# Optimization experiments

Measured on AMD Instinct MI355X. Metric: run time of the kernel, lower is better.

The kernel has to match this reference:

```python
import jax, jax.numpy as jnp
import numpy as np

D_MODEL, N_HEADS, D_FF = 768, 12, 3072
B, S = 2, 2048
EPS = 1e-6

def _ln(x, alpha, bias):
    # Matches torch: std with Bessel correction (unbiased), scalar alpha/bias
    mean = x.mean(axis=-1, keepdims=True)
    std = jnp.std(x, axis=-1, keepdims=True, ddof=1)
    return alpha * (x - mean) / (std + EPS) + bias

def setup_inputs() -> dict:
    key = jax.random.key(0)
    ks = jax.random.split(key, 12)
    def w(k, shp):
        return jax.random.normal(k, shp, dtype=jnp.float32) * 0.02
    inp = {
        "x": jax.random.normal(ks[0], (B, S, D_MODEL), dtype=jnp.float32),
        "mask": jnp.ones((B, 1, 1, S), dtype=jnp.int32),
        "wq": w(ks[1], (D_MODEL, D_MODEL)), "bq": jnp.zeros((D_MODEL,), jnp.float32),
        "wk": w(ks[2], (D_MODEL, D_MODEL)), "bk": jnp.zeros((D_MODEL,), jnp.float32),
        "wv": w(ks[3], (D_MODEL, D_MODEL)), "bv": jnp.zeros((D_MODEL,), jnp.float32),
        "wo": w(ks[4], (D_MODEL, D_MODEL)), "bo": jnp.zeros((D_MODEL,), jnp.float32),
        "w1": w(ks[5], (D_MODEL, D_FF)), "b1": jnp.zeros((D_FF,), jnp.float32),
        "w2": w(ks[6], (D_FF, D_MODEL)), "b2": jnp.zeros((D_MODEL,), jnp.float32),
        "ln1_a": jnp.ones((1,), jnp.float32), "ln1_b": jnp.zeros((1,), jnp.float32),
        "ln2_a": jnp.ones((1,), jnp.float32), "ln2_b": jnp.zeros((1,), jnp.float32),
    }
    return inp

def reference(x, mask, wq, bq, wk, bk, wv, bv, wo, bo, w1, b1, w2, b2,
              ln1_a, ln1_b, ln2_a, ln2_b):
    d_k = D_MODEL // N_HEADS
    # --- residual 1: pre-LN self-attention ---
    h = _ln(x, ln1_a, ln1_b)
    q = (h @ wq + bq).reshape(B, S, N_HEADS, d_k).transpose(0, 2, 1, 3)
    k = (h @ wk + bk).reshape(B, S, N_HEADS, d_k).transpose(0, 2, 1, 3)
    v = (h @ wv + bv).reshape(B, S, N_HEADS, d_k).transpose(0, 2, 1, 3)
    scores = jnp.einsum('bhqd,bhkd->bhqk', q, k) / jnp.sqrt(jnp.float32(d_k))
    scores = jnp.where(mask == 0, jnp.float32(-1e9), scores)
    attn = jax.nn.softmax(scores, axis=-1)            # [B,H,S,S] materialized, as in source
    ctx = jnp.einsum('bhqk,bhkd->bhqd', attn, v)
    ctx = ctx.transpose(0, 2, 1, 3).reshape(B, S, D_MODEL)
    x = x + (ctx @ wo + bo)
    # --- residual 2: pre-LN FFN ---
    h = _ln(x, ln2_a, ln2_b)
    ffn = jax.nn.relu(h @ w1 + b1) @ w2 + b2
    return x + ffn
```

## Files before the change

kernel.cpp:

```cpp
#include <hip/hip_runtime.h>
#include <math.h>

#define DM    768
#define NH    12
#define DKH   64
#define DFF   3072
#define BATCH 2
#define SLEN  2048
#define MTOT  4096
#define LNEPS 1e-6f
#define QSCALE 0.18033688011112042f

typedef unsigned short u16;
typedef __attribute__((ext_vector_type(8))) short bf16x8;
typedef __attribute__((ext_vector_type(4))) float f32x4;
typedef __attribute__((ext_vector_type(4))) unsigned short us4;

__device__ __forceinline__ u16 f2bf(float f) {
    union { float f; unsigned int u; } v; v.f = f;
    unsigned int r = v.u + 0x7FFFu + ((v.u >> 16) & 1u);
    return (u16)(r >> 16);
}

__device__ __forceinline__ unsigned pk2bf_t(float lo, float hi) {
    union { float f; unsigned u; } a, b;
    a.f = lo; b.f = hi;
    return __builtin_amdgcn_perm(b.u, a.u, 0x07060302u);
}

__device__ __forceinline__ void gld16(const void* g, void* lds) {
    __builtin_amdgcn_global_load_lds(
        (const __attribute__((address_space(1))) unsigned int*)(unsigned long long)g,
        (__attribute__((address_space(3))) unsigned int*)(unsigned int)(unsigned long long)lds,
        16, 0, 0);
}

__global__ __launch_bounds__(256) void ln_kernel(const float* __restrict__ x,
                                                 u16* __restrict__ out,
                                                 const float* __restrict__ alpha_p,
                                                 const float* __restrict__ beta_p,
                                                 const float* __restrict__ b2,
                                                 float* __restrict__ out2) {
    int row = blockIdx.x;
    const float* xr = x + (size_t)row * DM;
    int t = threadIdx.x;
    float v0 = xr[t], v1 = xr[t + 256], v2 = xr[t + 512];
    float s = v0 + v1 + v2;
    #pragma unroll
    for (int off = 32; off > 0; off >>= 1) s += __shfl_down(s, off);
    __shared__ float red[4], red2[4];
    int wv = t >> 6, ln = t & 63;
    if (ln == 0) red[wv] = s;
    __syncthreads();
    float mean = (red[0] + red[1] + red[2] + red[3]) * (1.0f / 768.0f);
    float d0 = v0 - mean, d1 = v1 - mean, d2 = v2 - mean;
    float sq = d0 * d0 + d1 * d1 + d2 * d2;
    #pragma unroll
    for (int off = 32; off > 0; off >>= 1) sq += __shfl_down(sq, off);
    if (ln == 0) red2[wv] = sq;
    __syncthreads();
    float var = (red2[0] + red2[1] + red2[2] + red2[3]) * (1.0f / 767.0f);
    float scale = alpha_p[0] / (sqrtf(var) + LNEPS);
    float bias = beta_p[0];
    u16* orow = out + (size_t)row * DM;
    orow[t]       = f2bf(d0 * scale + bias);
    orow[t + 256] = f2bf(d1 * scale + bias);
    orow[t + 512] = f2bf(d2 * scale + bias);
    if (out2) {
        float* o2 = out2 + (size_t)row * DM;
        o2[t]       = v0 + b2[t];
        o2[t + 256] = v1 + b2[t + 256];
        o2[t + 512] = v2 + b2[t + 512];
    }
}

__global__ __launch_bounds__(256) void wcast_all(
        const float* __restrict__ wq, const float* __restrict__ wk,
        const float* __restrict__ wv, const float* __restrict__ wo,
        const float* __restrict__ w1, const float* __restrict__ w2,
        u16* __restrict__ wqT, u16* __restrict__ wkT, u16* __restrict__ wvT,
        u16* __restrict__ woT, u16* __restrict__ w1T, u16* __restrict__ w2T) {
    __shared__ float tile[32][33];
    int bid = blockIdx.x;
    const float* src; u16* dst; int R, C, bx, by;
    if (bid < 2304) {
        int j = bid / 576, tix = bid % 576;
        R = 768; C = 768; bx = tix % 24; by = tix / 24;
        src = (j == 0) ? wq : (j == 1) ? wk : (j == 2) ? wv : wo;
        dst = (j == 0) ? wqT : (j == 1) ? wkT : (j == 2) ? wvT : woT;
    } else if (bid < 4608) {
        int tix = bid - 2304;
        R = 768; C = 3072; bx = tix % 96; by = tix / 96;
        src = w1; dst = w1T;
    } else {
        int tix = bid - 4608;
        R = 3072; C = 768; bx = tix % 24; by = tix / 24;
        src = w2; dst = w2T;
    }
    int t = threadIdx.x, tx = t & 31, ty = t >> 5;
    int r0 = by * 32, c0 = bx * 32;
    #pragma unroll
    for (int p = 0; p < 4; p++)
        tile[ty + p * 8][tx] = src[(size_t)(r0 + ty + p * 8) * C + c0 + tx];
    __syncthreads();
    #pragma unroll
    for (int p = 0; p < 4; p++)
        dst[(size_t)(c0 + ty + p * 8) * R + r0 + tx] = f2bf(tile[tx][ty + p * 8]);
}

template<int EPI>
__device__ __forceinline__ void gemm128_core(const u16* __restrict__ A,
                                             const u16* __restrict__ Wt,
                                             const float* __restrict__ bias,
                                             const float* __restrict__ resid,
                                             void* __restrict__ Cout,
                                             int M, int N, int Kstride, int Kloop,
                                             float scale, int bm, int bn) {
    __shared__ __align__(16) u16 As[2][128 * 32];
    __shared__ __align__(16) u16 Bs[2][128 * 32];
    int t = threadIdx.x;
    int ln = t & 63, w = t >> 6;
    int wm = w >> 1, wn = w & 1;
    int quad = ln >> 4, col = ln & 15;
    int m0 = bm * 128, n0 = bn * 128;

    f32x4 acc[4][4];
    const f32x4 zero = {0.f, 0.f, 0.f, 0.f};
    #pragma unroll
    for (int i = 0; i < 4; i++)
        #pragma unroll
        for (int j = 0; j < 4; j++) acc[i][j] = zero;

    int st_ch = (((ln & 3) ^ ((ln >> 3) & 3))) * 8;
    const u16* Ag = A  + (size_t)(m0 + 32 * w + (ln >> 2)) * Kstride + st_ch;
    const u16* Bg = Wt + (size_t)(n0 + 32 * w + (ln >> 2)) * Kstride + st_ch;

    gld16(Ag,                As[0] + w * 1024);
    gld16(Ag + 16 * Kstride, As[0] + w * 1024 + 512);
    gld16(Bg,                Bs[0] + w * 1024);
    gld16(Bg + 16 * Kstride, Bs[0] + w * 1024 + 512);
    __syncthreads();

    int rch = (quad ^ ((col >> 1) & 3)) * 8;

    for (int k0 = 0; k0 < Kloop; k0 += 32) {
        int cur = (k0 >> 5) & 1, nxt = cur ^ 1;
        if (k0 + 32 < Kloop) {
            gld16(Ag + k0 + 32,                As[nxt] + w * 1024);
            gld16(Ag + k0 + 32 + 16 * Kstride, As[nxt] + w * 1024 + 512);
            gld16(Bg + k0 + 32,                Bs[nxt] + w * 1024);
            gld16(Bg + k0 + 32 + 16 * Kstride, Bs[nxt] + w * 1024 + 512);
        }
        bf16x8 af[4], bfr[4];
        #pragma unroll
        for (int i = 0; i < 4; i++)
            af[i] = *(const bf16x8*)&As[cur][(wm * 64 + i * 16 + col) * 32 + rch];
        #pragma unroll
        for (int j = 0; j < 4; j++)
            bfr[j] = *(const bf16x8*)&Bs[cur][(wn * 64 + j * 16 + col) * 32 + rch];
        #pragma unroll
        for (int i = 0; i < 4; i++)
            #pragma unroll
            for (int j = 0; j < 4; j++)
                acc[i][j] = __builtin_amdgcn_mfma_f32_16x16x32_bf16(af[i], bfr[j], acc[i][j], 0, 0, 0);
        __syncthreads();
    }

    #pragma unroll
    for (int i = 0; i < 4; i++) {
        int mb = m0 + wm * 64 + i * 16 + quad * 4;
        #pragma unroll
        for (int j = 0; j < 4; j++) {
            int n = n0 + wn * 64 + j * 16 + col;
            if (EPI == 0 || EPI == 1) {
                float bs = bias[n];
                u16* Cb = (u16*)Cout;
                #pragma unroll
                for (int r = 0; r < 4; r++) {
                    float f = (acc[i][j][r] + bs) * ((EPI == 0) ? scale : 1.0f);
                    if (EPI == 1) f = fmaxf(f, 0.f);
                    Cb[(size_t)(mb + r) * N + n] = f2bf(f);
                }
            } else if (EPI == 2) {
                float bs = bias[n];
                float* Cf = (float*)Cout;
                #pragma unroll
                for (int r = 0; r < 4; r++)
                    Cf[(size_t)(mb + r) * N + n] =
                        acc[i][j][r] + bs + resid[(size_t)(mb + r) * N + n];
            } else if (EPI == 3) {
                float bs = bias[n];
                u16* Cb = (u16*)Cout;
                us4 pk;
                #pragma unroll
                for (int r = 0; r < 4; r++) pk[r] = f2bf(acc[i][j][r] + bs);
                *(us4*)&Cb[(size_t)n * M + mb] = pk;
            } else {
                float* Cf = (float*)Cout;
                #pragma unroll
                for (int r = 0; r < 4; r++)
                    atomicAdd(&Cf[(size_t)(mb + r) * N + n], acc[i][j][r]);
            }
        }
    }
}

template<int EPI>
__global__ __launch_bounds__(256) void gemm_kernel(const u16* __restrict__ A,
                                                   const u16* __restrict__ Wt,
                                                   const float* __restrict__ bias,
                                                   const float* __restrict__ resid,
                                                   void* __restrict__ C,
                                                   int M, int N, int Kstride, int Kloop,
                                                   float scale) {
    const u16* Az = A  + (size_t)blockIdx.z * Kloop;
    const u16* Wz = Wt + (size_t)blockIdx.z * Kloop;
    gemm128_core<EPI>(Az, Wz, bias, resid, C, M, N, Kstride, Kloop, scale,
                      blockIdx.y, blockIdx.x);
}

__global__ __launch_bounds__(256) void qkv_kernel(const u16* __restrict__ h,
        const u16* __restrict__ wqT, const u16* __restrict__ wkT, const u16* __restrict__ wvT,
        const float* __restrict__ bq, const float* __restrict__ bk, const float* __restrict__ bv,
        u16* __restrict__ q, u16* __restrict__ k, u16* __restrict__ vT) {
    int z = blockIdx.z;
    if (z == 0)      gemm128_core<0>(h, wqT, bq, nullptr, q,  MTOT, DM, DM, DM, QSCALE, blockIdx.y, blockIdx.x);
    else if (z == 1) gemm128_core<0>(h, wkT, bk, nullptr, k,  MTOT, DM, DM, DM, 1.0f,   blockIdx.y, blockIdx.x);
    else             gemm128_core<3>(h, wvT, bv, nullptr, vT, MTOT, DM, DM, DM, 1.0f,   blockIdx.y, blockIdx.x);
}

template<int EPI>
__global__ __launch_bounds__(256) void gemm64_kernel(const u16* __restrict__ A,
                                                     const u16* __restrict__ Wt,
                                                     const float* __restrict__ bias,
                                                     const float* __restrict__ resid,
                                                     void* __restrict__ Cout,
                                                     int M, int N, int Kstride, int Kloop) {
    __shared__ __align__(16) u16 As[2][64 * 32];
    __shared__ __align__(16) u16 Bs[2][64 * 32];
    int t = threadIdx.x, ln = t & 63, w = t >> 6;
    int wm = w >> 1, wn = w & 1;
    int quad = ln >> 4, col = ln & 15;
    int m0 = blockIdx.y * 64, n0 = blockIdx.x * 64;

    f32x4 acc[2][2];
    const f32x4 zero = {0.f, 0.f, 0.f, 0.f};
    #pragma unroll
    for (int i = 0; i < 2; i++)
        #pragma unroll
        for (int j = 0; j < 2; j++) acc[i][j] = zero;

    int st_ch = (((ln & 3) ^ ((ln >> 3) & 3))) * 8;
    const u16* Ag = A  + (size_t)(m0 + 16 * w + (ln >> 2)) * Kstride + st_ch;
    const u16* Bg = Wt + (size_t)(n0 + 16 * w + (ln >> 2)) * Kstride + st_ch;
    gld16(Ag, As[0] + w * 512);
    gld16(Bg, Bs[0] + w * 512);
    __syncthreads();

    int rch = (quad ^ ((col >> 1) & 3)) * 8;

    for (int k0 = 0; k0 < Kloop; k0 += 32) {
        int cur = (k0 >> 5) & 1, nxt = cur ^ 1;
        if (k0 + 32 < Kloop) {
            gld16(Ag + k0 + 32, As[nxt] + w * 512);
            gld16(Bg + k0 + 32, Bs[nxt] + w * 512);
        }
        bf16x8 af[2], bfr[2];
        #pragma unroll
        for (int i = 0; i < 2; i++)
            af[i] = *(const bf16x8*)&As[cur][(wm * 32 + i * 16 + col) * 32 + rch];
        #pragma unroll
        for (int j = 0; j < 2; j++)
            bfr[j] = *(const bf16x8*)&Bs[cur][(wn * 32 + j * 16 + col) * 32 + rch];
        #pragma unroll
        for (int i = 0; i < 2; i++)
            #pragma unroll
            for (int j = 0; j < 2; j++)
                acc[i][j] = __builtin_amdgcn_mfma_f32_16x16x32_bf16(af[i], bfr[j], acc[i][j], 0, 0, 0);
        __syncthreads();
    }

    #pragma unroll
    for (int i = 0; i < 2; i++) {
        int mb = m0 + wm * 32 + i * 16 + quad * 4;
        #pragma unroll
        for (int j = 0; j < 2; j++) {
            int n = n0 + wn * 32 + j * 16 + col;
            float bs = bias[n];
            float* Cf = (float*)Cout;
            #pragma unroll
            for (int r = 0; r < 4; r++)
                Cf[(size_t)(mb + r) * N + n] =
                    acc[i][j][r] + bs + resid[(size_t)(mb + r) * N + n];
        }
    }
}

__global__ __launch_bounds__(256) void attn_kernel(const u16* __restrict__ qg,
                                                   const u16* __restrict__ kg,
                                                   const u16* __restrict__ vTg,
                                                   const int* __restrict__ mask,
                                                   u16* __restrict__ ctx) {
    __shared__ __align__(16) u16 Qs[64 * 64];
    __shared__ __align__(16) u16 KV[4][64 * 64];
    __shared__ __align__(16) u16 Ps[4][32 * 40];
    __shared__ __align__(16) float Msf[2][64];
    __shared__ float Lp[64][2];
    int t = threadIdx.x, ln = t & 63, w = t >> 6;
    int quad = ln >> 4, col = ln & 15;
    int qh = w >> 1, kh = w & 1;
    int bh = blockIdx.x, qb = blockIdx.y;
    int b = bh / NH, h = bh - b * NH;
    int q0 = qb * 64;
    size_t qkbase = ((size_t)b * SLEN) * DM + h * DKH;
    size_t vbase  = ((size_t)h * DKH) * MTOT + (size_t)b * SLEN;

    int sw_st = (((ln & 7) ^ (ln >> 3)) * 8);

    {
        const u16* g0 = qg + qkbase + (size_t)(q0 + 16 * w + (ln >> 3)) * DM + sw_st;
        gld16(g0,          Qs + w * 1024);
        gld16(g0 + 8 * DM, Qs + w * 1024 + 512);
        const u16* kg0 = kg + qkbase + (size_t)(16 * w + (ln >> 3)) * DM + sw_st;
        gld16(kg0,          KV[0] + w * 1024);
        gld16(kg0 + 8 * DM, KV[0] + w * 1024 + 512);
        const u16* vg0 = vTg + vbase + (size_t)(16 * w + (ln >> 3)) * MTOT + sw_st;
        gld16(vg0,            KV[2] + w * 1024);
        gld16(vg0 + 8 * MTOT, KV[2] + w * 1024 + 512);
        if (t < 64) Msf[0][t] = mask[b * SLEN + t] ? 0.f : -1e9f;
    }
    __syncthreads();

    bf16x8 bqf[2][2];
    #pragma unroll
    for (int qgi = 0; qgi < 2; qgi++) {
        int rq = qh * 32 + qgi * 16 + col;
        int cq = ((quad ^ (rq & 7)) * 8);
        bqf[qgi][0] = *(const bf16x8*)&Qs[rq * 64 + cq];
        bqf[qgi][1] = *(const bf16x8*)&Qs[rq * 64 + (cq ^ 32)];
    }

    const u16* kpn = kg + qkbase + (size_t)(64 + 16 * w + (ln >> 3)) * DM + sw_st;
    const u16* vpn = vTg + vbase + (size_t)(16 * w + (ln >> 3)) * MTOT + 64 + sw_st;
    const int* mpn = mask + b * SLEN + 64 + t;

    float lacc[2] = {0.f, 0.f};
    f32x4 Ov[2][4];
    const f32x4 zero = {0.f, 0.f, 0.f, 0.f};
    #pragma unroll
    for (int qgi = 0; qgi < 2; qgi++)
        #pragma unroll
        for (int dg = 0; dg < 4; dg++) Ov[qgi][dg] = zero;
    u16* Psw = &Ps[w][0];

    for (int j0 = 0; j0 < SLEN; j0 += 64) {
        int cur = (j0 >> 6) & 1, nxt = cur ^ 1;
        if (j0 + 64 < SLEN) {
            gld16(kpn,            KV[nxt] + w * 1024);
            gld16(kpn + 8 * DM,   KV[nxt] + w * 1024 + 512);
            gld16(vpn,            KV[2 + nxt] + w * 1024);
            gld16(vpn + 8 * MTOT, KV[2 + nxt] + w * 1024 + 512);
            if (t < 64) Msf[nxt][t] = *mpn ? 0.f : -1e9f;
            kpn += 64 * DM; vpn += 64; mpn += 64;
        }

        bf16x8 ak[2][2];
        #pragma unroll
        for (int kgi = 0; kgi < 2; kgi++) {
            int rk = kh * 32 + kgi * 16 + col;
            int ck = ((quad ^ (rk & 7)) * 8);
            ak[kgi][0] = *(const bf16x8*)&KV[cur][rk * 64 + ck];
            ak[kgi][1] = *(const bf16x8*)&KV[cur][rk * 64 + (ck ^ 32)];
        }
        #pragma unroll
        for (int kgi = 0; kgi < 2; kgi++) {
            f32x4 bias4 = *(const f32x4*)&Msf[cur][kh * 32 + kgi * 16 + quad * 4];
            #pragma unroll
            for (int qgi = 0; qgi < 2; qgi++) {
                f32x4 S = __builtin_amdgcn_mfma_f32_16x16x32_bf16(ak[kgi][0], bqf[qgi][0], bias4, 0, 0, 0);
                S       = __builtin_amdgcn_mfma_f32_16x16x32_bf16(ak[kgi][1], bqf[qgi][1], S,     0, 0, 0);
                float p0 = exp2f(S[0]), p1 = exp2f(S[1]);
                float p2 = exp2f(S[2]), p3 = exp2f(S[3]);
                lacc[qgi] += (p0 + p1) + (p2 + p3);
                uint2 pk;
                pk.x = pk2bf_t(p0, p1);
                pk.y = pk2bf_t(p2, p3);
                *(uint2*)&Psw[(qgi * 16 + col) * 40 + kgi * 16 + quad * 4] = pk;
            }
        }
        bf16x8 ap[2];
        #pragma unroll
        for (int qgi = 0; qgi < 2; qgi++)
            ap[qgi] = *(const bf16x8*)&Psw[(qgi * 16 + col) * 40 + quad * 8];
        #pragma unroll
        for (int dg = 0; dg < 4; dg++) {
            int rv = dg * 16 + col;
            int cv = (((kh * 4 + quad) ^ (rv & 7)) * 8);
            bf16x8 bv = *(const bf16x8*)&KV[2 + cur][rv * 64 + cv];
            Ov[0][dg] = __builtin_amdgcn_mfma_f32_16x16x32_bf16(ap[0], bv, Ov[0][dg], 0, 0, 0);
            Ov[1][dg] = __builtin_amdgcn_mfma_f32_16x16x32_bf16(ap[1], bv, Ov[1][dg], 0, 0, 0);
        }
        __syncthreads();
    }

    #pragma unroll
    for (int qgi = 0; qgi < 2; qgi++) {
        lacc[qgi] += __shfl_xor(lacc[qgi], 16);
        lacc[qgi] += __shfl_xor(lacc[qgi], 32);
        if (quad == 0) Lp[qh * 32 + qgi * 16 + col][kh] = lacc[qgi];
    }
    float* Osh = (float*)&KV[0][0];
    if (kh == 1) {
        #pragma unroll
        for (int qgi = 0; qgi < 2; qgi++)
            #pragma unroll
            for (int dg = 0; dg < 4; dg++)
                *(f32x4*)&Osh[(qh * 64 + dg * 16 + col) * 36 + qgi * 16 + quad * 4] = Ov[qgi][dg];
    }
    __syncthreads();
    if (kh == 0) {
        #pragma unroll
        for (int qgi = 0; qgi < 2; qgi++) {
            float linv[4];
            #pragma unroll
            for (int r = 0; r < 4; r++) {
                int ql = qh * 32 + qgi * 16 + quad * 4 + r;
                linv[r] = 1.0f / (Lp[ql][0] + Lp[ql][1]);
            }
            #pragma unroll
            for (int dg = 0; dg < 4; dg++) {
                f32x4 oo = *(const f32x4*)&Osh[(qh * 64 + dg * 16 + col) * 36 + qgi * 16 + quad * 4];
                #pragma unroll
                for (int r = 0; r < 4; r++) {
                    int qrow = q0 + qh * 32 + qgi * 16 + quad * 4 + r;
                    ctx[qkbase + (size_t)qrow * DM + dg * 16 + col] =
                        f2bf((Ov[qgi][dg][r] + oo[r]) * linv[r]);
                }
            }
        }
    }
}

extern "C" void kernel_launch(void* const* d_in, const int* in_sizes, int n_in,
                              void* d_out, int out_size, void* d_ws, size_t ws_size,
                              hipStream_t stream) {
    const float* x    = (const float*)d_in[0];
    const int*   mask = (const int*)d_in[1];
    const float* wq   = (const float*)d_in[2];
    const float* bq   = (const float*)d_in[3];
    const float* wk   = (const float*)d_in[4];
    const float* bk   = (const float*)d_in[5];
    const float* wv   = (const float*)d_in[6];
    const float* bv   = (const float*)d_in[7];
    const float* wo   = (const float*)d_in[8];
    const float* bo   = (const float*)d_in[9];
    const float* w1   = (const float*)d_in[10];
    const float* b1   = (const float*)d_in[11];
    const float* w2   = (const float*)d_in[12];
    const float* b2   = (const float*)d_in[13];
    const float* ln1a = (const float*)d_in[14];
    const float* ln1b = (const float*)d_in[15];
    const float* ln2a = (const float*)d_in[16];
    const float* ln2b = (const float*)d_in[17];
    float* out = (float*)d_out;

    char* w8 = (char*)d_ws;
    u16*   ffn = (u16*)(w8 + 0);
    u16*   q   = (u16*)(w8 + 0);
    u16*   kb  = (u16*)(w8 + 6291456);
    u16*   vT  = (u16*)(w8 + 12582912);
    u16*   ctx = (u16*)(w8 + 18874368);
    u16*   h   = (u16*)(w8 + 25165824);
    float* x1  = (float*)(w8 + 31457280);
    u16*   wqT = (u16*)(w8 + 44040192);
    u16*   wkT = (u16*)(w8 + 45219840);
    u16*   wvT = (u16*)(w8 + 46399488);
    u16*   woT = (u16*)(w8 + 47579136);
    u16*   w1T = (u16*)(w8 + 48758784);
    u16*   w2T = (u16*)(w8 + 53477376);

    wcast_all<<<6912, 256, 0, stream>>>(wq, wk, wv, wo, w1, w2,
                                        wqT, wkT, wvT, woT, w1T, w2T);
    ln_kernel<<<MTOT, 256, 0, stream>>>(x, h, ln1a, ln1b, nullptr, nullptr);
    qkv_kernel<<<dim3(6, 32, 3), 256, 0, stream>>>(h, wqT, wkT, wvT, bq, bk, bv, q, kb, vT);
    attn_kernel<<<dim3(BATCH * NH, SLEN / 64), 256, 0, stream>>>(q, kb, vT, mask, ctx);
    gemm64_kernel<2><<<dim3(12, 64), 256, 0, stream>>>(ctx, woT, bo, x, (void*)x1,
                                                       MTOT, DM, DM, DM);
    ln_kernel<<<MTOT, 256, 0, stream>>>(x1, h, ln2a, ln2b, b2, out);
    gemm_kernel<1><<<dim3(24, 32), 256, 0, stream>>>(h, w1T, b1, nullptr, (void*)ffn,
                                                     MTOT, DFF, DM, DM, 1.0f);
    gemm_kernel<5><<<dim3(6, 32, 2), 256, 0, stream>>>(ffn, w2T, nullptr, nullptr, (void*)out,
                                                       MTOT, DM, DFF, DFF / 2, 1.0f);
}
```

Measured before the change: 294.6 us.

## Shrink all GEMM tiles to 64x64, fuse LN1 into weight prep, MFMA row sums

Replaces the 128x128 GEMM core with a 64x64 core for the QKV, FFN1 and FFN2 GEMMs, quadrupling block counts to raise occupancy and CU coverage at the cost of lower per-block data reuse. Merges the first LayerNorm launch into the weight-cast kernel to save a launch. In attention, the softmax denominator is accumulated with an MFMA against a ones vector instead of scalar adds and shuffles, offloading VALU work onto the matrix unit.

```diff
diff --git a/kernel.cpp b/kernel.cpp
--- a/kernel.cpp
+++ b/kernel.cpp
@@ -35,13 +35,12 @@
         16, 0, 0);
 }
 
-__global__ __launch_bounds__(256) void ln_kernel(const float* __restrict__ x,
-                                                 u16* __restrict__ out,
-                                                 const float* __restrict__ alpha_p,
-                                                 const float* __restrict__ beta_p,
-                                                 const float* __restrict__ b2,
-                                                 float* __restrict__ out2) {
-    int row = blockIdx.x;
+__device__ __forceinline__ void ln_body(const float* __restrict__ x,
+                                        u16* __restrict__ out,
+                                        const float* __restrict__ alpha_p,
+                                        const float* __restrict__ beta_p,
+                                        const float* __restrict__ b2,
+                                        float* __restrict__ out2, int row) {
     const float* xr = x + (size_t)row * DM;
     int t = threadIdx.x;
     float v0 = xr[t], v1 = xr[t + 256], v2 = xr[t + 512];
@@ -74,14 +73,44 @@
     }
 }
 
-__global__ __launch_bounds__(256) void wcast_all(
+__global__ __launch_bounds__(256) void ln_kernel(const float* __restrict__ x,
+                                                 u16* __restrict__ out,
+                                                 const float* __restrict__ alpha_p,
+                                                 const float* __restrict__ beta_p,
+                                                 const float* __restrict__ b2,
+                                                 float* __restrict__ out2) {
+    ln_body(x, out, alpha_p, beta_p, b2, out2, blockIdx.x);
+}
+
+__device__ __forceinline__ void wcast_body(const float* __restrict__ src,
+                                           u16* __restrict__ dst,
+                                           int R, int C, int bx, int by) {
+    __shared__ float tile[32][33];
+    int t = threadIdx.x, tx = t & 31, ty = t >> 5;
+    int r0 = by * 32, c0 = bx * 32;
+    #pragma unroll
+    for (int p = 0; p < 4; p++)
+        tile[ty + p * 8][tx] = src[(size_t)(r0 + ty + p * 8) * C + c0 + tx];
+    __syncthreads();
+    #pragma unroll
+    for (int p = 0; p < 4; p++)
+        dst[(size_t)(c0 + ty + p * 8) * R + r0 + tx] = f2bf(tile[tx][ty + p * 8]);
+}
+
+__global__ __launch_bounds__(256) void prep_kernel(
+        const float* __restrict__ x, u16* __restrict__ h,
+        const float* __restrict__ ln1a, const float* __restrict__ ln1b,
         const float* __restrict__ wq, const float* __restrict__ wk,
         const float* __restrict__ wv, const float* __restrict__ wo,
         const float* __restrict__ w1, const float* __restrict__ w2,
         u16* __restrict__ wqT, u16* __restrict__ wkT, u16* __restrict__ wvT,
         u16* __restrict__ woT, u16* __restrict__ w1T, u16* __restrict__ w2T) {
-    __shared__ float tile[32][33];
     int bid = blockIdx.x;
+    if (bid < MTOT) {
+        ln_body(x, h, ln1a, ln1b, nullptr, nullptr, bid);
+        return;
+    }
+    bid -= MTOT;
     const float* src; u16* dst; int R, C, bx, by;
     if (bid < 2304) {
         int j = bid / 576, tix = bid % 576;
@@ -97,48 +126,36 @@
         R = 3072; C = 768; bx = tix % 24; by = tix / 24;
         src = w2; dst = w2T;
     }
-    int t = threadIdx.x, tx = t & 31, ty = t >> 5;
-    int r0 = by * 32, c0 = bx * 32;
-    #pragma unroll
-    for (int p = 0; p < 4; p++)
-        tile[ty + p * 8][tx] = src[(size_t)(r0 + ty + p * 8) * C + c0 + tx];
-    __syncthreads();
-    #pragma unroll
-    for (int p = 0; p < 4; p++)
-        dst[(size_t)(c0 + ty + p * 8) * R + r0 + tx] = f2bf(tile[tx][ty + p * 8]);
+    wcast_body(src, dst, R, C, bx, by);
 }
 
 template<int EPI>
-__device__ __forceinline__ void gemm128_core(const u16* __restrict__ A,
-                                             const u16* __restrict__ Wt,
-                                             const float* __restrict__ bias,
-                                             const float* __restrict__ resid,
-                                             void* __restrict__ Cout,
-                                             int M, int N, int Kstride, int Kloop,
-                                             float scale, int bm, int bn) {
-    __shared__ __align__(16) u16 As[2][128 * 32];
-    __shared__ __align__(16) u16 Bs[2][128 * 32];
-    int t = threadIdx.x;
-    int ln = t & 63, w = t >> 6;
+__device__ __forceinline__ void gemm64_core(const u16* __restrict__ A,
+                                            const u16* __restrict__ Wt,
+                                            const float* __restrict__ bias,
+                                            const float* __restrict__ resid,
+                                            void* __restrict__ Cout,
+                                            int M, int N, int Kstride, int Kloop,
+                                            float scale, int bm, int bn) {
+    __shared__ __align__(16) u16 As[2][64 * 32];
+    __shared__ __align__(16) u16 Bs[2][64 * 32];
+    int t = threadIdx.x, ln = t & 63, w = t >> 6;
     int wm = w >> 1, wn = w & 1;
     int quad = ln >> 4, col = ln & 15;
-    int m0 = bm * 128, n0 = bn * 128;
-
-    f32x4 acc[4][4];
+    int m0 = bm * 64, n0 = bn * 64;
+
+    f32x4 acc[2][2];
     const f32x4 zero = {0.f, 0.f, 0.f, 0.f};
     #pragma unroll
-    for (int i = 0; i < 4; i++)
-        #pragma unroll
-        for (int j = 0; j < 4; j++) acc[i][j] = zero;
+    for (int i = 0; i < 2; i++)
+        #pragma unroll
+        for (int j = 0; j < 2; j++) acc[i][j] = zero;
 
     int st_ch = (((ln & 3) ^ ((ln >> 3) & 3))) * 8;
-    const u16* Ag = A  + (size_t)(m0 + 32 * w + (ln >> 2)) * Kstride + st_ch;
-    const u16* Bg = Wt + (size_t)(n0 + 32 * w + (ln >> 2)) * Kstride + st_ch;
-
-    gld16(Ag,                As[0] + w * 1024);
-    gld16(Ag + 16 * Kstride, As[0] + w * 1024 + 512);
-    gld16(Bg,                Bs[0] + w * 1024);
-    gld16(Bg + 16 * Kstride, Bs[0] + w * 1024 + 512);
+    const u16* Ag = A  + (size_t)(m0 + 16 * w + (ln >> 2)) * Kstride + st_ch;
+    const u16* Bg = Wt + (size_t)(n0 + 16 * w + (ln >> 2)) * Kstride + st_ch;
+    gld16(Ag, As[0] + w * 512);
+    gld16(Bg, Bs[0] + w * 512);
     __syncthreads();
 
     int rch = (quad ^ ((col >> 1) & 3)) * 8;
@@ -146,32 +163,30 @@
     for (int k0 = 0; k0 < Kloop; k0 += 32) {
         int cur = (k0 >> 5) & 1, nxt = cur ^ 1;
         if (k0 + 32 < Kloop) {
-            gld16(Ag + k0 + 32,                As[nxt] + w * 1024);
-            gld16(Ag + k0 + 32 + 16 * Kstride, As[nxt] + w * 1024 + 512);
-            gld16(Bg + k0 + 32,                Bs[nxt] + w * 1024);
-            gld16(Bg + k0 + 32 + 16 * Kstride, Bs[nxt] + w * 1024 + 512);
-        }
-        bf16x8 af[4], bfr[4];
-        #pragma unroll
-        for (int i = 0; i < 4; i++)
-            af[i] = *(const bf16x8*)&As[cur][(wm * 64 + i * 16 + col) * 32 + rch];
-        #pragma unroll
-        for (int j = 0; j < 4; j++)
-            bfr[j] = *(const bf16x8*)&Bs[cur][(wn * 64 + j * 16 + col) * 32 + rch];
-        #pragma unroll
-        for (int i = 0; i < 4; i++)
+            gld16(Ag + k0 + 32, As[nxt] + w * 512);
+            gld16(Bg + k0 + 32, Bs[nxt] + w * 512);
+        }
+        bf16x8 af[2], bfr[2];
+        #pragma unroll
+        for (int i = 0; i < 2; i++)
+            af[i] = *(const bf16x8*)&As[cur][(wm * 32 + i * 16 + col) * 32 + rch];
+        #pragma unroll
+        for (int j = 0; j < 2; j++)
+            bfr[j] = *(const bf16x8*)&Bs[cur][(wn * 32 + j * 16 + col) * 32 + rch];
+        #pragma unroll
+        for (int i = 0; i < 2; i++)
             #pragma unroll
-            for (int j = 0; j < 4; j++)
+            for (int j = 0; j < 2; j++)
                 acc[i][j] = __builtin_amdgcn_mfma_f32_16x16x32_bf16(af[i], bfr[j], acc[i][j], 0, 0, 0);
         __syncthreads();
     }
 
     #pragma unroll
-    for (int i = 0; i < 4; i++) {
-        int mb = m0 + wm * 64 + i * 16 + quad * 4;
-        #pragma unroll
-        for (int j = 0; j < 4; j++) {
-            int n = n0 + wn * 64 + j * 16 + col;
+    for (int i = 0; i < 2; i++) {
+        int mb = m0 + wm * 32 + i * 16 + quad * 4;
+        #pragma unroll
+        for (int j = 0; j < 2; j++) {
+            int n = n0 + wn * 32 + j * 16 + col;
             if (EPI == 0 || EPI == 1) {
                 float bs = bias[n];
                 u16* Cb = (u16*)Cout;
@@ -206,17 +221,17 @@
 }
 
 template<int EPI>
-__global__ __launch_bounds__(256) void gemm_kernel(const u16* __restrict__ A,
-                                                   const u16* __restrict__ Wt,
-                                                   const float* __restrict__ bias,
-                                                   const float* __restrict__ resid,
-                                                   void* __restrict__ C,
-                                                   int M, int N, int Kstride, int Kloop,
-                                                   float scale) {
+__global__ __launch_bounds__(256) void gemm64_kernel(const u16* __restrict__ A,
+                                                     const u16* __restrict__ Wt,
+                                                     const float* __restrict__ bias,
+                                                     const float* __restrict__ resid,
+                                                     void* __restrict__ C,
+                                                     int M, int N, int Kstride, int Kloop,
+                                                     float scale) {
     const u16* Az = A  + (size_t)blockIdx.z * Kloop;
     const u16* Wz = Wt + (size_t)blockIdx.z * Kloop;
-    gemm128_core<EPI>(Az, Wz, bias, resid, C, M, N, Kstride, Kloop, scale,
-                      blockIdx.y, blockIdx.x);
+    gemm64_core<EPI>(Az, Wz, bias, resid, C, M, N, Kstride, Kloop, scale,
+                     blockIdx.y, blockIdx.x);
 }
 
 __global__ __launch_bounds__(256) void qkv_kernel(const u16* __restrict__ h,
@@ -224,76 +239,9 @@
         const float* __restrict__ bq, const float* __restrict__ bk, const float* __restrict__ bv,
         u16* __restrict__ q, u16* __restrict__ k, u16* __restrict__ vT) {
     int z = blockIdx.z;
-    if (z == 0)      gemm128_core<0>(h, wqT, bq, nullptr, q,  MTOT, DM, DM, DM, QSCALE, blockIdx.y, blockIdx.x);
-    else if (z == 1) gemm128_core<0>(h, wkT, bk, nullptr, k,  MTOT, DM, DM, DM, 1.0f,   blockIdx.y, blockIdx.x);
-    else             gemm128_core<3>(h, wvT, bv, nullptr, vT, MTOT, DM, DM, DM, 1.0f,   blockIdx.y, blockIdx.x);
-}
-
-template<int EPI>
-__global__ __launch_bounds__(256) void gemm64_kernel(const u16* __restrict__ A,
-                                                     const u16* __restrict__ Wt,
-                                                     const float* __restrict__ bias,
-                                                     const float* __restrict__ resid,
-                                                     void* __restrict__ Cout,
-                                                     int M, int N, int Kstride, int Kloop) {
-    __shared__ __align__(16) u16 As[2][64 * 32];
-    __shared__ __align__(16) u16 Bs[2][64 * 32];
-    int t = threadIdx.x, ln = t & 63, w = t >> 6;
-    int wm = w >> 1, wn = w & 1;
-    int quad = ln >> 4, col = ln & 15;
-    int m0 = blockIdx.y * 64, n0 = blockIdx.x * 64;
-
-    f32x4 acc[2][2];
-    const f32x4 zero = {0.f, 0.f, 0.f, 0.f};
-    #pragma unroll
-    for (int i = 0; i < 2; i++)
-        #pragma unroll
-        for (int j = 0; j < 2; j++) acc[i][j] = zero;
-
-    int st_ch = (((ln & 3) ^ ((ln >> 3) & 3))) * 8;
-    const u16* Ag = A  + (size_t)(m0 + 16 * w + (ln >> 2)) * Kstride + st_ch;
-    const u16* Bg = Wt + (size_t)(n0 + 16 * w + (ln >> 2)) * Kstride + st_ch;
-    gld16(Ag, As[0] + w * 512);
-    gld16(Bg, Bs[0] + w * 512);
-    __syncthreads();
-
-    int rch = (quad ^ ((col >> 1) & 3)) * 8;
-
-    for (int k0 = 0; k0 < Kloop; k0 += 32) {
-        int cur = (k0 >> 5) & 1, nxt = cur ^ 1;
-        if (k0 + 32 < Kloop) {
-            gld16(Ag + k0 + 32, As[nxt] + w * 512);
-            gld16(Bg + k0 + 32, Bs[nxt] + w * 512);
-        }
-        bf16x8 af[2], bfr[2];
-        #pragma unroll
-        for (int i = 0; i < 2; i++)
-            af[i] = *(const bf16x8*)&As[cur][(wm * 32 + i * 16 + col) * 32 + rch];
-        #pragma unroll
-        for (int j = 0; j < 2; j++)
-            bfr[j] = *(const bf16x8*)&Bs[cur][(wn * 32 + j * 16 + col) * 32 + rch];
-        #pragma unroll
-        for (int i = 0; i < 2; i++)
-            #pragma unroll
-            for (int j = 0; j < 2; j++)
-                acc[i][j] = __builtin_amdgcn_mfma_f32_16x16x32_bf16(af[i], bfr[j], acc[i][j], 0, 0, 0);
-        __syncthreads();
-    }
-
-    #pragma unroll
-    for (int i = 0; i < 2; i++) {
-        int mb = m0 + wm * 32 + i * 16 + quad * 4;
-        #pragma unroll
-        for (int j = 0; j < 2; j++) {
-            int n = n0 + wn * 32 + j * 16 + col;
-            float bs = bias[n];
-            float* Cf = (float*)Cout;
-            #pragma unroll
-            for (int r = 0; r < 4; r++)
-                Cf[(size_t)(mb + r) * N + n] =
-                    acc[i][j][r] + bs + resid[(size_t)(mb + r) * N + n];
-        }
-    }
+    if (z == 0)      gemm64_core<0>(h, wqT, bq, nullptr, q,  MTOT, DM, DM, DM, QSCALE, blockIdx.y, blockIdx.x);
+    else if (z == 1) gemm64_core<0>(h, wkT, bk, nullptr, k,  MTOT, DM, DM, DM, 1.0f,   blockIdx.y, blockIdx.x);
+    else             gemm64_core<3>(h, wvT, bv, nullptr, vT, MTOT, DM, DM, DM, 1.0f,   blockIdx.y, blockIdx.x);
 }
 
 __global__ __launch_bounds__(256) void attn_kernel(const u16* __restrict__ qg,
@@ -305,7 +253,7 @@
     __shared__ __align__(16) u16 KV[4][64 * 64];
     __shared__ __align__(16) u16 Ps[4][32 * 40];
     __shared__ __align__(16) float Msf[2][64];
-    __shared__ float Lp[64][2];
+    __shared__ float Lp[64];
     int t = threadIdx.x, ln = t & 63, w = t >> 6;
     int quad = ln >> 4, col = ln & 15;
     int qh = w >> 1, kh = w & 1;
@@ -340,17 +288,22 @@
         bqf[qgi][1] = *(const bf16x8*)&Qs[rq * 64 + (cq ^ 32)];
     }
 
+    bf16x8 vones;
+    #pragma unroll
+    for (int i = 0; i < 8; i++) vones[i] = (short)0x3F80;
+
     const u16* kpn = kg + qkbase + (size_t)(64 + 16 * w + (ln >> 3)) * DM + sw_st;
     const u16* vpn = vTg + vbase + (size_t)(16 * w + (ln >> 3)) * MTOT + 64 + sw_st;
     const int* mpn = mask + b * SLEN + 64 + t;
 
-    float lacc[2] = {0.f, 0.f};
-    f32x4 Ov[2][4];
+    f32x4 Ov[2][4], Lv[2];
     const f32x4 zero = {0.f, 0.f, 0.f, 0.f};
     #pragma unroll
-    for (int qgi = 0; qgi < 2; qgi++)
+    for (int qgi = 0; qgi < 2; qgi++) {
+        Lv[qgi] = zero;
         #pragma unroll
         for (int dg = 0; dg < 4; dg++) Ov[qgi][dg] = zero;
+    }
     u16* Psw = &Ps[w][0];
 
     for (int j0 = 0; j0 < SLEN; j0 += 64) {
@@ -381,7 +334,6 @@
                 S       = __builtin_amdgcn_mfma_f32_16x16x32_bf16(ak[kgi][1], bqf[qgi][1], S,     0, 0, 0);
                 float p0 = exp2f(S[0]), p1 = exp2f(S[1]);
                 float p2 = exp2f(S[2]), p3 = exp2f(S[3]);
-                lacc[qgi] += (p0 + p1) + (p2 + p3);
                 uint2 pk;
                 pk.x = pk2bf_t(p0, p1);
                 pk.y = pk2bf_t(p2, p3);
@@ -390,8 +342,10 @@
         }
         bf16x8 ap[2];
         #pragma unroll
-        for (int qgi = 0; qgi < 2; qgi++)
+        for (int qgi = 0; qgi < 2; qgi++) {
             ap[qgi] = *(const bf16x8*)&Psw[(qgi * 16 + col) * 40 + quad * 8];
+            Lv[qgi] = __builtin_amdgcn_mfma_f32_16x16x32_bf16(ap[qgi], vones, Lv[qgi], 0, 0, 0);
+        }
         #pragma unroll
         for (int dg = 0; dg < 4; dg++) {
             int rv = dg * 16 + col;
@@ -403,19 +357,19 @@
         __syncthreads();
     }
 
-    #pragma unroll
-    for (int qgi = 0; qgi < 2; qgi++) {
-        lacc[qgi] += __shfl_xor(lacc[qgi], 16);
-        lacc[qgi] += __shfl_xor(lacc[qgi], 32);
-        if (quad == 0) Lp[qh * 32 + qgi * 16 + col][kh] = lacc[qgi];
-    }
     float* Osh = (float*)&KV[0][0];
     if (kh == 1) {
         #pragma unroll
-        for (int qgi = 0; qgi < 2; qgi++)
+        for (int qgi = 0; qgi < 2; qgi++) {
             #pragma unroll
             for (int dg = 0; dg < 4; dg++)
                 *(f32x4*)&Osh[(qh * 64 + dg * 16 + col) * 36 + qgi * 16 + quad * 4] = Ov[qgi][dg];
+            if (col == 0) {
+                #pragma unroll
+                for (int r = 0; r < 4; r++)
+                    Lp[qh * 32 + qgi * 16 + quad * 4 + r] = Lv[qgi][r];
+            }
+        }
     }
     __syncthreads();
     if (kh == 0) {
@@ -425,7 +379,7 @@
             #pragma unroll
             for (int r = 0; r < 4; r++) {
                 int ql = qh * 32 + qgi * 16 + quad * 4 + r;
-                linv[r] = 1.0f / (Lp[ql][0] + Lp[ql][1]);
+                linv[r] = 1.0f / (Lv[qgi][r] + Lp[ql]);
             }
             #pragma unroll
             for (int dg = 0; dg < 4; dg++) {
@@ -479,16 +433,16 @@
     u16*   w1T = (u16*)(w8 + 48758784);
     u16*   w2T = (u16*)(w8 + 53477376);
 
-    wcast_all<<<6912, 256, 0, stream>>>(wq, wk, wv, wo, w1, w2,
-                                        wqT, wkT, wvT, woT, w1T, w2T);
-    ln_kernel<<<MTOT, 256, 0, stream>>>(x, h, ln1a, ln1b, nullptr, nullptr);
-    qkv_kernel<<<dim3(6, 32, 3), 256, 0, stream>>>(h, wqT, wkT, wvT, bq, bk, bv, q, kb, vT);
+    prep_kernel<<<MTOT + 6912, 256, 0, stream>>>(x, h, ln1a, ln1b,
+                                                 wq, wk, wv, wo, w1, w2,
+                                                 wqT, wkT, wvT, woT, w1T, w2T);
+    qkv_kernel<<<dim3(12, 64, 3), 256, 0, stream>>>(h, wqT, wkT, wvT, bq, bk, bv, q, kb, vT);
     attn_kernel<<<dim3(BATCH * NH, SLEN / 64), 256, 0, stream>>>(q, kb, vT, mask, ctx);
     gemm64_kernel<2><<<dim3(12, 64), 256, 0, stream>>>(ctx, woT, bo, x, (void*)x1,
-                                                       MTOT, DM, DM, DM);
+                                                       MTOT, DM, DM, DM, 1.0f);
     ln_kernel<<<MTOT, 256, 0, stream>>>(x1, h, ln2a, ln2b, b2, out);
-    gemm_kernel<1><<<dim3(24, 32), 256, 0, stream>>>(h, w1T, b1, nullptr, (void*)ffn,
-                                                     MTOT, DFF, DM, DM, 1.0f);
-    gemm_kernel<5><<<dim3(6, 32, 2), 256, 0, stream>>>(ffn, w2T, nullptr, nullptr, (void*)out,
-                                                       MTOT, DM, DFF, DFF / 2, 1.0f);
-}
+    gemm64_kernel<1><<<dim3(48, 64), 256, 0, stream>>>(h, w1T, b1, nullptr, (void*)ffn,
+                                                       MTOT, DFF, DM, DM, 1.0f);
+    gemm64_kernel<5><<<dim3(12, 64, 2), 256, 0, stream>>>(ffn, w2T, nullptr, nullptr, (void*)out,
+                                                          MTOT, DM, DFF, DFF / 2, 1.0f);
+}
```

Measured after the change: 330.1 us. +12.0%, slower.

## Remap GEMM blocks per XCD, merge LN1 with weight cast, compute softmax sum via MFMA

Applied to the files above, without the earlier changes.

Adds an XCD-aware block-index mapping to all GEMM launches, so blocks sharing the same A rows land on the same XCD and reuse its L2. The first LayerNorm is folded into the weight-cast kernel, which saves one launch. In attention, the softmax row sums are now computed with an extra MFMA against a ones vector instead of scalar adds plus shuffles. The MFMA sum uses bf16-rounded probabilities rather than the fp32 values, which slightly changes the numerics.

```diff
diff --git a/kernel.cpp b/kernel.cpp
--- a/kernel.cpp
+++ b/kernel.cpp
@@ -35,13 +35,18 @@
         16, 0, 0);
 }
 
-__global__ __launch_bounds__(256) void ln_kernel(const float* __restrict__ x,
-                                                 u16* __restrict__ out,
-                                                 const float* __restrict__ alpha_p,
-                                                 const float* __restrict__ beta_p,
-                                                 const float* __restrict__ b2,
-                                                 float* __restrict__ out2) {
-    int row = blockIdx.x;
+__device__ __forceinline__ void xcd_map(int id, int Nb, int& bm, int& bn) {
+    int xcd = id & 7, loc = id >> 3;
+    bn = loc % Nb;
+    bm = (loc / Nb) * 8 + xcd;
+}
+
+__device__ __forceinline__ void ln_body(const float* __restrict__ x,
+                                        u16* __restrict__ out,
+                                        const float* __restrict__ alpha_p,
+                                        const float* __restrict__ beta_p,
+                                        const float* __restrict__ b2,
+                                        float* __restrict__ out2, int row) {
     const float* xr = x + (size_t)row * DM;
     int t = threadIdx.x;
     float v0 = xr[t], v1 = xr[t + 256], v2 = xr[t + 512];
@@ -74,14 +79,44 @@
     }
 }
 
-__global__ __launch_bounds__(256) void wcast_all(
+__global__ __launch_bounds__(256) void ln_kernel(const float* __restrict__ x,
+                                                 u16* __restrict__ out,
+                                                 const float* __restrict__ alpha_p,
+                                                 const float* __restrict__ beta_p,
+                                                 const float* __restrict__ b2,
+                                                 float* __restrict__ out2) {
+    ln_body(x, out, alpha_p, beta_p, b2, out2, blockIdx.x);
+}
+
+__device__ __forceinline__ void wcast_body(const float* __restrict__ src,
+                                           u16* __restrict__ dst,
+                                           int R, int C, int bx, int by) {
+    __shared__ float tile[32][33];
+    int t = threadIdx.x, tx = t & 31, ty = t >> 5;
+    int r0 = by * 32, c0 = bx * 32;
+    #pragma unroll
+    for (int p = 0; p < 4; p++)
+        tile[ty + p * 8][tx] = src[(size_t)(r0 + ty + p * 8) * C + c0 + tx];
+    __syncthreads();
+    #pragma unroll
+    for (int p = 0; p < 4; p++)
+        dst[(size_t)(c0 + ty + p * 8) * R + r0 + tx] = f2bf(tile[tx][ty + p * 8]);
+}
+
+__global__ __launch_bounds__(256) void prep_kernel(
+        const float* __restrict__ x, u16* __restrict__ h,
+        const float* __restrict__ ln1a, const float* __restrict__ ln1b,
         const float* __restrict__ wq, const float* __restrict__ wk,
         const float* __restrict__ wv, const float* __restrict__ wo,
         const float* __restrict__ w1, const float* __restrict__ w2,
         u16* __restrict__ wqT, u16* __restrict__ wkT, u16* __restrict__ wvT,
         u16* __restrict__ woT, u16* __restrict__ w1T, u16* __restrict__ w2T) {
-    __shared__ float tile[32][33];
     int bid = blockIdx.x;
+    if (bid < MTOT) {
+        ln_body(x, h, ln1a, ln1b, nullptr, nullptr, bid);
+        return;
+    }
+    bid -= MTOT;
     const float* src; u16* dst; int R, C, bx, by;
     if (bid < 2304) {
         int j = bid / 576, tix = bid % 576;
@@ -97,15 +132,7 @@
         R = 3072; C = 768; bx = tix % 24; by = tix / 24;
         src = w2; dst = w2T;
     }
-    int t = threadIdx.x, tx = t & 31, ty = t >> 5;
-    int r0 = by * 32, c0 = bx * 32;
-    #pragma unroll
-    for (int p = 0; p < 4; p++)
-        tile[ty + p * 8][tx] = src[(size_t)(r0 + ty + p * 8) * C + c0 + tx];
-    __syncthreads();
-    #pragma unroll
-    for (int p = 0; p < 4; p++)
-        dst[(size_t)(c0 + ty + p * 8) * R + r0 + tx] = f2bf(tile[tx][ty + p * 8]);
+    wcast_body(src, dst, R, C, bx, by);
 }
 
 template<int EPI>
@@ -212,11 +239,12 @@
                                                    const float* __restrict__ resid,
                                                    void* __restrict__ C,
                                                    int M, int N, int Kstride, int Kloop,
-                                                   float scale) {
+                                                   float scale, int Nb) {
     const u16* Az = A  + (size_t)blockIdx.z * Kloop;
     const u16* Wz = Wt + (size_t)blockIdx.z * Kloop;
-    gemm128_core<EPI>(Az, Wz, bias, resid, C, M, N, Kstride, Kloop, scale,
-                      blockIdx.y, blockIdx.x);
+    int bm, bn;
+    xcd_map(blockIdx.x, Nb, bm, bn);
+    gemm128_core<EPI>(Az, Wz, bias, resid, C, M, N, Kstride, Kloop, scale, bm, bn);
 }
 
 __global__ __launch_bounds__(256) void qkv_kernel(const u16* __restrict__ h,
@@ -224,9 +252,11 @@
         const float* __restrict__ bq, const float* __restrict__ bk, const float* __restrict__ bv,
         u16* __restrict__ q, u16* __restrict__ k, u16* __restrict__ vT) {
     int z = blockIdx.z;
-    if (z == 0)      gemm128_core<0>(h, wqT, bq, nullptr, q,  MTOT, DM, DM, DM, QSCALE, blockIdx.y, blockIdx.x);
-    else if (z == 1) gemm128_core<0>(h, wkT, bk, nullptr, k,  MTOT, DM, DM, DM, 1.0f,   blockIdx.y, blockIdx.x);
-    else             gemm128_core<3>(h, wvT, bv, nullptr, vT, MTOT, DM, DM, DM, 1.0f,   blockIdx.y, blockIdx.x);
+    int bm, bn;
+    xcd_map(blockIdx.x, 6, bm, bn);
+    if (z == 0)      gemm128_core<0>(h, wqT, bq, nullptr, q,  MTOT, DM, DM, DM, QSCALE, bm, bn);
+    else if (z == 1) gemm128_core<0>(h, wkT, bk, nullptr, k,  MTOT, DM, DM, DM, 1.0f,   bm, bn);
+    else             gemm128_core<3>(h, wvT, bv, nullptr, vT, MTOT, DM, DM, DM, 1.0f,   bm, bn);
 }
 
 template<int EPI>
@@ -235,13 +265,16 @@
                                                      const float* __restrict__ bias,
                                                      const float* __restrict__ resid,
                                                      void* __restrict__ Cout,
-                                                     int M, int N, int Kstride, int Kloop) {
+                                                     int M, int N, int Kstride, int Kloop,
+                                                     int Nb) {
     __shared__ __align__(16) u16 As[2][64 * 32];
     __shared__ __align__(16) u16 Bs[2][64 * 32];
     int t = threadIdx.x, ln = t & 63, w = t >> 6;
     int wm = w >> 1, wn = w & 1;
     int quad = ln >> 4, col = ln & 15;
-    int m0 = blockIdx.y * 64, n0 = blockIdx.x * 64;
+    int bm, bn;
+    xcd_map(blockIdx.x, Nb, bm, bn);
+    int m0 = bm * 64, n0 = bn * 64;
 
     f32x4 acc[2][2];
     const f32x4 zero = {0.f, 0.f, 0.f, 0.f};
@@ -305,7 +338,7 @@
     __shared__ __align__(16) u16 KV[4][64 * 64];
     __shared__ __align__(16) u16 Ps[4][32 * 40];
     __shared__ __align__(16) float Msf[2][64];
-    __shared__ float Lp[64][2];
+    __shared__ float Lp[64];
     int t = threadIdx.x, ln = t & 63, w = t >> 6;
     int quad = ln >> 4, col = ln & 15;
     int qh = w >> 1, kh = w & 1;
@@ -340,17 +373,22 @@
         bqf[qgi][1] = *(const bf16x8*)&Qs[rq * 64 + (cq ^ 32)];
     }
 
+    bf16x8 vones;
+    #pragma unroll
+    for (int i = 0; i < 8; i++) vones[i] = (short)0x3F80;
+
     const u16* kpn = kg + qkbase + (size_t)(64 + 16 * w + (ln >> 3)) * DM + sw_st;
     const u16* vpn = vTg + vbase + (size_t)(16 * w + (ln >> 3)) * MTOT + 64 + sw_st;
     const int* mpn = mask + b * SLEN + 64 + t;
 
-    float lacc[2] = {0.f, 0.f};
-    f32x4 Ov[2][4];
+    f32x4 Ov[2][4], Lv[2];
     const f32x4 zero = {0.f, 0.f, 0.f, 0.f};
     #pragma unroll
-    for (int qgi = 0; qgi < 2; qgi++)
+    for (int qgi = 0; qgi < 2; qgi++) {
+        Lv[qgi] = zero;
         #pragma unroll
         for (int dg = 0; dg < 4; dg++) Ov[qgi][dg] = zero;
+    }
     u16* Psw = &Ps[w][0];
 
     for (int j0 = 0; j0 < SLEN; j0 += 64) {
@@ -381,7 +419,6 @@
                 S       = __builtin_amdgcn_mfma_f32_16x16x32_bf16(ak[kgi][1], bqf[qgi][1], S,     0, 0, 0);
                 float p0 = exp2f(S[0]), p1 = exp2f(S[1]);
                 float p2 = exp2f(S[2]), p3 = exp2f(S[3]);
-                lacc[qgi] += (p0 + p1) + (p2 + p3);
                 uint2 pk;
                 pk.x = pk2bf_t(p0, p1);
                 pk.y = pk2bf_t(p2, p3);
@@ -390,8 +427,10 @@
         }
         bf16x8 ap[2];
         #pragma unroll
-        for (int qgi = 0; qgi < 2; qgi++)
+        for (int qgi = 0; qgi < 2; qgi++) {
             ap[qgi] = *(const bf16x8*)&Psw[(qgi * 16 + col) * 40 + quad * 8];
+            Lv[qgi] = __builtin_amdgcn_mfma_f32_16x16x32_bf16(ap[qgi], vones, Lv[qgi], 0, 0, 0);
+        }
         #pragma unroll
         for (int dg = 0; dg < 4; dg++) {
             int rv = dg * 16 + col;
@@ -403,19 +442,19 @@
         __syncthreads();
     }
 
-    #pragma unroll
-    for (int qgi = 0; qgi < 2; qgi++) {
-        lacc[qgi] += __shfl_xor(lacc[qgi], 16);
-        lacc[qgi] += __shfl_xor(lacc[qgi], 32);
-        if (quad == 0) Lp[qh * 32 + qgi * 16 + col][kh] = lacc[qgi];
-    }
     float* Osh = (float*)&KV[0][0];
     if (kh == 1) {
         #pragma unroll
-        for (int qgi = 0; qgi < 2; qgi++)
+        for (int qgi = 0; qgi < 2; qgi++) {
             #pragma unroll
             for (int dg = 0; dg < 4; dg++)
                 *(f32x4*)&Osh[(qh * 64 + dg * 16 + col) * 36 + qgi * 16 + quad * 4] = Ov[qgi][dg];
+            if (col == 0) {
+                #pragma unroll
+                for (int r = 0; r < 4; r++)
+                    Lp[qh * 32 + qgi * 16 + quad * 4 + r] = Lv[qgi][r];
+            }
+        }
     }
     __syncthreads();
     if (kh == 0) {
@@ -425,7 +464,7 @@
             #pragma unroll
             for (int r = 0; r < 4; r++) {
                 int ql = qh * 32 + qgi * 16 + quad * 4 + r;
-                linv[r] = 1.0f / (Lp[ql][0] + Lp[ql][1]);
+                linv[r] = 1.0f / (Lv[qgi][r] + Lp[ql]);
             }
             #pragma unroll
             for (int dg = 0; dg < 4; dg++) {
@@ -479,16 +518,16 @@
     u16*   w1T = (u16*)(w8 + 48758784);
     u16*   w2T = (u16*)(w8 + 53477376);
 
-    wcast_all<<<6912, 256, 0, stream>>>(wq, wk, wv, wo, w1, w2,
-                                        wqT, wkT, wvT, woT, w1T, w2T);
-    ln_kernel<<<MTOT, 256, 0, stream>>>(x, h, ln1a, ln1b, nullptr, nullptr);
-    qkv_kernel<<<dim3(6, 32, 3), 256, 0, stream>>>(h, wqT, wkT, wvT, bq, bk, bv, q, kb, vT);
+    prep_kernel<<<MTOT + 6912, 256, 0, stream>>>(x, h, ln1a, ln1b,
+                                                 wq, wk, wv, wo, w1, w2,
+                                                 wqT, wkT, wvT, woT, w1T, w2T);
+    qkv_kernel<<<dim3(192, 1, 3), 256, 0, stream>>>(h, wqT, wkT, wvT, bq, bk, bv, q, kb, vT);
     attn_kernel<<<dim3(BATCH * NH, SLEN / 64), 256, 0, stream>>>(q, kb, vT, mask, ctx);
-    gemm64_kernel<2><<<dim3(12, 64), 256, 0, stream>>>(ctx, woT, bo, x, (void*)x1,
-                                                       MTOT, DM, DM, DM);
+    gemm64_kernel<2><<<768, 256, 0, stream>>>(ctx, woT, bo, x, (void*)x1,
+                                              MTOT, DM, DM, DM, 12);
     ln_kernel<<<MTOT, 256, 0, stream>>>(x1, h, ln2a, ln2b, b2, out);
-    gemm_kernel<1><<<dim3(24, 32), 256, 0, stream>>>(h, w1T, b1, nullptr, (void*)ffn,
-                                                     MTOT, DFF, DM, DM, 1.0f);
-    gemm_kernel<5><<<dim3(6, 32, 2), 256, 0, stream>>>(ffn, w2T, nullptr, nullptr, (void*)out,
-                                                       MTOT, DM, DFF, DFF / 2, 1.0f);
-}
+    gemm_kernel<1><<<768, 256, 0, stream>>>(h, w1T, b1, nullptr, (void*)ffn,
+                                            MTOT, DFF, DM, DM, 1.0f, 24);
+    gemm_kernel<5><<<dim3(192, 1, 2), 256, 0, stream>>>(ffn, w2T, nullptr, nullptr, (void*)out,
+                                                        MTOT, DM, DFF, DFF / 2, 1.0f, 6);
+}
```

After: 285.7 us. 3.0% less time.
